# Optimization experiments

Measured on AMD Instinct MI355X. Metric: run time of the kernel, lower is better.

## Reference

```python
import jax, jax.numpy as jnp
import numpy as np

NUM_HEADS = 8  # matches init_kwargs num_heads
LN_EPS = 1e-5  # torch.nn.LayerNorm default


def setup_inputs() -> dict:
    key = jax.random.key(0)
    ks = jax.random.split(key, 12)
    E, B, H, S = 16384, 16, 256, 32
    edge_features = jax.random.normal(ks[0], (E, H), jnp.float32)
    edge_coords = jax.random.normal(ks[1], (E, 3), jnp.float32)
    # sorted, equal-size segments (all graphs non-empty)
    batch = jnp.repeat(jnp.arange(B, dtype=jnp.int32), E // B)
    s_h = 1.0 / np.sqrt(H)
    s_sh = 1.0 / np.sqrt(S * H)
    seed_vectors = jax.random.normal(ks[2], (S, H), jnp.float32)
    # weights stored [in, out] (transposed vs torch nn.Linear)
    Wq = jax.random.normal(ks[3], (H, H), jnp.float32) * s_h
    Wk = jax.random.normal(ks[4], (H, H), jnp.float32) * s_h
    Wv = jax.random.normal(ks[5], (H, H), jnp.float32) * s_h
    Wo = jax.random.normal(ks[6], (H, H), jnp.float32) * s_h
    bo = jnp.zeros((H,), jnp.float32)
    ln_g = jnp.ones((H,), jnp.float32)
    ln_b = jnp.zeros((H,), jnp.float32)
    W1 = jax.random.normal(ks[7], (S * H, H), jnp.float32) * s_sh
    b1 = jnp.zeros((H,), jnp.float32)
    W2 = jax.random.normal(ks[8], (H, H), jnp.float32) * s_h
    b2 = jnp.zeros((H,), jnp.float32)
    return dict(edge_features=edge_features, edge_coords=edge_coords, batch=batch,
                seed_vectors=seed_vectors, Wq=Wq, Wk=Wk, Wv=Wv, Wo=Wo, bo=bo,
                ln_g=ln_g, ln_b=ln_b, W1=W1, b1=b1, W2=W2, b2=b2, num_graphs=B)


def reference(edge_features, edge_coords, batch, seed_vectors, Wq, Wk, Wv, Wo, bo,
              ln_g, ln_b, W1, b1, W2, b2, num_graphs):
    S, H = seed_vectors.shape
    nh = NUM_HEADS
    hd = H // nh
    q = (seed_vectors @ Wq).reshape(S, nh, hd)          # shared across graphs
    k = (edge_features @ Wk).reshape(-1, nh, hd)        # [E, nh, hd]
    v = (edge_features @ Wv).reshape(-1, nh, hd)
    scores = jnp.einsum('shd,ehd->esh', q, k) / np.sqrt(hd).astype(np.float32)
    # segment softmax over edges within each graph
    m = jax.lax.stop_gradient(jax.ops.segment_max(scores, batch, num_segments=num_graphs))
    num = jnp.exp(scores - m[batch])
    den = jax.ops.segment_sum(num, batch, num_segments=num_graphs)
    w = num / den[batch]                                # [E, S, nh]
    att = jax.ops.segment_sum(jnp.einsum('esh,ehd->eshd', w, v), batch,
                              num_segments=num_graphs)  # [B, S, nh, hd]
    att = att.reshape(num_graphs, S, H)                 # concat heads (head-major)
    y = seed_vectors[None, :, :] + att @ Wo + bo        # residual + out_proj
    mu = jnp.mean(y, axis=-1, keepdims=True)
    var = jnp.mean((y - mu) ** 2, axis=-1, keepdims=True)
    y = (y - mu) / jnp.sqrt(var + LN_EPS) * ln_g + ln_b
    flat = y.reshape(num_graphs, S * H)
    h1 = jax.nn.silu(flat @ W1 + b1)
    return h1 @ W2 + b2                                 # [B, H]
```

## Files before the change

### kernel.cpp

```cpp
#include <hip/hip_runtime.h>
#include <math.h>
#include <stdint.h>

#define E_EDGES 16384
#define H_DIM   256
#define S_SEEDS 32
#define NHEADS  8
#define HDIM    32
#define BGRAPHS 16
#define EPG     1024
#define NCHUNK  256
#define CPG     16
#define RSQRT_HD 0.17677669529663687f

typedef __attribute__((ext_vector_type(8))) short bf16x8;
typedef __attribute__((ext_vector_type(4))) float f32x4;

__device__ inline unsigned short f2bf(float x) {
    unsigned u = __float_as_uint(x);
    u += 0x7fff + ((u >> 16) & 1);
    return (unsigned short)(u >> 16);
}
__device__ inline float bf2f(unsigned int h) {
    return __uint_as_float((h & 0xffffu) << 16);
}
__device__ inline unsigned pack2(float a, float b) {
    return (unsigned)f2bf(a) | ((unsigned)f2bf(b) << 16);
}

__global__ __launch_bounds__(256) void k_wc(const float* __restrict__ Wv,
                                            const float* __restrict__ Wk,
                                            const float* __restrict__ Wq,
                                            const float* __restrict__ seed,
                                            unsigned short* __restrict__ WcT) {
    int j = blockIdx.x;
    int i = threadIdx.x;
    float val;
    if (j < H_DIM) {
        val = Wv[i * H_DIM + j];
    } else {
        int c = j - H_DIM;
        int h = c >> 5, s = c & 31;
        __shared__ float qp[8][33];
        __shared__ float qrow[HDIM];
        int d = i & 31, g = i >> 5;
        const float* wq = &Wq[(g * 32) * H_DIM + h * HDIM + d];
        const float* sd = &seed[s * H_DIM + g * 32];
        float p = 0.f;
        #pragma unroll
        for (int ii = 0; ii < 32; ++ii)
            p = fmaf(sd[ii], wq[(size_t)ii * H_DIM], p);
        qp[g][d] = p;
        __syncthreads();
        if (i < HDIM) {
            float qv = 0.f;
            #pragma unroll
            for (int g2 = 0; g2 < 8; ++g2) qv += qp[g2][i];
            qrow[i] = qv;
        }
        __syncthreads();
        const float* wk = &Wk[i * H_DIM + h * HDIM];
        float acc = 0.f;
        #pragma unroll
        for (int dd = 0; dd < HDIM; dd += 4) {
            float4 w = *(const float4*)&wk[dd];
            float4 qq = *(const float4*)&qrow[dd];
            acc = fmaf(w.x, qq.x, acc); acc = fmaf(w.y, qq.y, acc);
            acc = fmaf(w.z, qq.z, acc); acc = fmaf(w.w, qq.w, acc);
        }
        val = acc * RSQRT_HD;
    }
    WcT[j * H_DIM + i] = f2bf(val);
}

struct HalfBuf {
    union {
        unsigned short Bs[2][128][40];
        unsigned short Pt[128][72];
    };
};
struct SMattn {
    unsigned short As[64][264];
    HalfBuf hb[2];
    unsigned short Vt[2][128][72];
    float smx[2][2][128];
    float ssm[2][2][128];
};

__global__ __launch_bounds__(512) void k_attn(const float* __restrict__ A,
                                              const unsigned short* __restrict__ WcT,
                                              float* __restrict__ outc,
                                              float* __restrict__ mg,
                                              float* __restrict__ sg) {
    __shared__ SMattn sm;
    int tid = threadIdx.x;
    int chunk = blockIdx.x;
    int e0 = chunk * 64;
    int half = tid >> 8;
    int tl = tid & 255;
    int w4 = tl >> 6, lane = tid & 63;
    int lr = lane & 15, kg = lane >> 4;
    int wm = (w4 & 1) * 32, wn = (w4 >> 1) * 64;

    {
        int r = tid >> 3, cg8 = tid & 7;
        const float* ap = &A[(size_t)(e0 + r) * H_DIM + cg8 * 32];
        #pragma unroll
        for (int i = 0; i < 4; ++i) {
            float4 x = *(const float4*)&ap[i * 8];
            float4 y = *(const float4*)&ap[i * 8 + 4];
            uint4 o;
            o.x = pack2(x.x, x.y); o.y = pack2(x.z, x.w);
            o.z = pack2(y.x, y.y); o.w = pack2(y.z, y.w);
            *(uint4*)&sm.As[r][cg8 * 32 + i * 8] = o;
        }
    }
    int brow = tl >> 1, bhalf16 = (tl & 1) * 16;
    f32x4 acc2[2][2] = {};
    uint4 pb0, pb1;
    {
        const unsigned short* bp = &WcT[(size_t)(half * 128 + brow) * H_DIM + bhalf16];
        pb0 = *(const uint4*)bp; pb1 = *(const uint4*)(bp + 8);
    }
    #pragma unroll
    for (int t2 = 0; t2 < 2; ++t2) {
        f32x4 acc[2][4] = {};
        #pragma unroll
        for (int k = 0; k < 8; ++k) {
            *(uint4*)&sm.hb[half].Bs[k & 1][brow][bhalf16]     = pb0;
            *(uint4*)&sm.hb[half].Bs[k & 1][brow][bhalf16 + 8] = pb1;
            __syncthreads();
            int nk = k + 1, nt2 = t2;
            if (nk == 8) { nk = 0; nt2 = t2 + 1; }
            if (nt2 < 2) {
                const unsigned short* bp =
                    &WcT[(size_t)(half * 128 + nt2 * 256 + brow) * H_DIM + nk * 32 + bhalf16];
                pb0 = *(const uint4*)bp; pb1 = *(const uint4*)(bp + 8);
            }
            bf16x8 af[2], bfv[4];
            #pragma unroll
            for (int mi = 0; mi < 2; ++mi)
                af[mi] = *(const bf16x8*)&sm.As[wm + mi * 16 + lr][k * 32 + kg * 8];
            #pragma unroll
            for (int ni = 0; ni < 4; ++ni)
                bfv[ni] = *(const bf16x8*)&sm.hb[half].Bs[k & 1][wn + ni * 16 + lr][kg * 8];
            #pragma unroll
            for (int mi = 0; mi < 2; ++mi)
                #pragma unroll
                for (int ni = 0; ni < 4; ++ni)
                    acc[mi][ni] = __builtin_amdgcn_mfma_f32_16x16x32_bf16(
                        af[mi], bfv[ni], acc[mi][ni], 0, 0, 0);
        }
        if (t2 == 0) {
            #pragma unroll
            for (int mi = 0; mi < 2; ++mi)
                #pragma unroll
                for (int ni = 0; ni < 4; ++ni)
                    #pragma unroll
                    for (int r = 0; r < 4; ++r)
                        sm.Vt[half][wn + ni * 16 + lr][wm + mi * 16 + kg * 4 + r] =
                            f2bf(acc[mi][ni][r]);
        } else {
            float tmax[4];
            #pragma unroll
            for (int ni = 0; ni < 4; ++ni) {
                float m = -1e30f;
                #pragma unroll
                for (int mi = 0; mi < 2; ++mi)
                    #pragma unroll
                    for (int r = 0; r < 4; ++r) m = fmaxf(m, acc[mi][ni][r]);
                m = fmaxf(m, __shfl_xor(m, 16, 64));
                m = fmaxf(m, __shfl_xor(m, 32, 64));
                tmax[ni] = m;
            }
            if (kg == 0) {
                #pragma unroll
                for (int ni = 0; ni < 4; ++ni)
                    sm.smx[half][w4 & 1][wn + ni * 16 + lr] = tmax[ni];
            }
            __syncthreads();
            float tsum[4];
            #pragma unroll
            for (int ni = 0; ni < 4; ++ni) {
                int col = wn + ni * 16 + lr;
                float m = fmaxf(sm.smx[half][0][col], sm.smx[half][1][col]);
                float sv = 0.f;
                #pragma unroll
                for (int mi = 0; mi < 2; ++mi)
                    #pragma unroll
                    for (int r = 0; r < 4; ++r) {
                        float e_ = __expf(acc[mi][ni][r] - m);
                        unsigned short eb = f2bf(e_);
                        sm.hb[half].Pt[col][wm + mi * 16 + kg * 4 + r] = eb;
                        sv += bf2f(eb);
                    }
                sv += __shfl_xor(sv, 16, 64);
                sv += __shfl_xor(sv, 32, 64);
                tsum[ni] = sv;
            }
            if (kg == 0) {
                #pragma unroll
                for (int ni = 0; ni < 4; ++ni)
                    sm.ssm[half][w4 & 1][wn + ni * 16 + lr] = tsum[ni];
            }
            __syncthreads();
            if (tl < 128) {
                float m = fmaxf(sm.smx[half][0][tl], sm.smx[half][1][tl]);
                float sv = sm.ssm[half][0][tl] + sm.ssm[half][1][tl];
                mg[(size_t)chunk * H_DIM + half * 128 + tl] = m;
                sg[(size_t)chunk * H_DIM + half * 128 + tl] = sv;
            }
            #pragma unroll
            for (int ms = 0; ms < 2; ++ms)
                #pragma unroll
                for (int nd = 0; nd < 2; ++nd)
                    #pragma unroll
                    for (int kk = 0; kk < 2; ++kk) {
                        bf16x8 pa = *(const bf16x8*)
                            &sm.hb[half].Pt[w4 * 32 + ms * 16 + lr][kk * 32 + kg * 8];
                        bf16x8 vb = *(const bf16x8*)
                            &sm.Vt[half][w4 * 32 + nd * 16 + lr][kk * 32 + kg * 8];
                        acc2[ms][nd] = __builtin_amdgcn_mfma_f32_16x16x32_bf16(
                            pa, vb, acc2[ms][nd], 0, 0, 0);
                    }
        }
    }
    #pragma unroll
    for (int ms = 0; ms < 2; ++ms)
        #pragma unroll
        for (int nd = 0; nd < 2; ++nd)
            #pragma unroll
            for (int r = 0; r < 4; ++r) {
                int s_ = ms * 16 + kg * 4 + r;
                int c_ = (half * 4 + w4) * 32 + nd * 16 + lr;
                outc[((size_t)chunk * 32 + s_) * H_DIM + c_] = acc2[ms][nd][r];
            }
}

__device__ inline float block_sum256(float v, float* red4) {
    for (int o = 32; o > 0; o >>= 1) v += __shfl_xor(v, o, 64);
    int wid = threadIdx.x >> 6;
    if ((threadIdx.x & 63) == 0) red4[wid] = v;
    __syncthreads();
    float r = red4[0] + red4[1] + red4[2] + red4[3];
    __syncthreads();
    return r;
}

__global__ __launch_bounds__(256) void k_proj_ln(const float* __restrict__ outc,
                                                 const float* __restrict__ mg,
                                                 const float* __restrict__ sg,
                                                 const float* __restrict__ seed,
                                                 const float* __restrict__ Wo,
                                                 const float* __restrict__ bo,
                                                 const float* __restrict__ ln_g,
                                                 const float* __restrict__ ln_b,
                                                 float* __restrict__ Y) {
    int bs0 = blockIdx.x * 4;
    int c = threadIdx.x;
    int b = bs0 >> 5;
    __shared__ float sscale[4][CPG][8];
    __shared__ float arow[4][H_DIM];
    __shared__ float red4[4];
    if (c < 32) {
        int r = c >> 3, hh = c & 7;
        int s_r = (bs0 + r) & 31;
        int sc = hh * 32 + s_r;
        float mj[CPG];
        float M = -1e30f;
        #pragma unroll
        for (int j = 0; j < CPG; ++j) {
            mj[j] = mg[(size_t)(b * CPG + j) * H_DIM + sc];
            M = fmaxf(M, mj[j]);
        }
        float Den = 0.f;
        #pragma unroll
        for (int j = 0; j < CPG; ++j)
            Den += sg[(size_t)(b * CPG + j) * H_DIM + sc] * __expf(mj[j] - M);
        float inv = 1.f / Den;
        #pragma unroll
        for (int j = 0; j < CPG; ++j)
            sscale[r][j][hh] = __expf(mj[j] - M) * inv;
    }
    __syncthreads();
    int h = c >> 5;
    #pragma unroll
    for (int r = 0; r < 4; ++r) {
        int s_r = (bs0 + r) & 31;
        float a = 0.f;
        #pragma unroll
        for (int j = 0; j < CPG; ++j)
            a = fmaf(outc[((size_t)(b * CPG + j) * 32 + s_r) * H_DIM + c],
                     sscale[r][j][h], a);
        arow[r][c] = a;
    }
    __syncthreads();
    float acc[4];
    float b0 = bo[c];
    #pragma unroll
    for (int r = 0; r < 4; ++r) acc[r] = b0;
    for (int i = 0; i < H_DIM; i += 4) {
        float4 a0 = *(const float4*)&arow[0][i];
        float4 a1 = *(const float4*)&arow[1][i];
        float4 a2 = *(const float4*)&arow[2][i];
        float4 a3 = *(const float4*)&arow[3][i];
        float w0 = Wo[(i + 0) * H_DIM + c], w1 = Wo[(i + 1) * H_DIM + c];
        float w2 = Wo[(i + 2) * H_DIM + c], w3 = Wo[(i + 3) * H_DIM + c];
        acc[0] = fmaf(a0.x, w0, acc[0]); acc[0] = fmaf(a0.y, w1, acc[0]);
        acc[0] = fmaf(a0.z, w2, acc[0]); acc[0] = fmaf(a0.w, w3, acc[0]);
        acc[1] = fmaf(a1.x, w0, acc[1]); acc[1] = fmaf(a1.y, w1, acc[1]);
        acc[1] = fmaf(a1.z, w2, acc[1]); acc[1] = fmaf(a1.w, w3, acc[1]);
        acc[2] = fmaf(a2.x, w0, acc[2]); acc[2] = fmaf(a2.y, w1, acc[2]);
        acc[2] = fmaf(a2.z, w2, acc[2]); acc[2] = fmaf(a2.w, w3, acc[2]);
        acc[3] = fmaf(a3.x, w0, acc[3]); acc[3] = fmaf(a3.y, w1, acc[3]);
        acc[3] = fmaf(a3.z, w2, acc[3]); acc[3] = fmaf(a3.w, w3, acc[3]);
    }
    float g = ln_g[c], be = ln_b[c];
    #pragma unroll
    for (int r = 0; r < 4; ++r) {
        int bs = bs0 + r;
        float y = seed[(bs & 31) * H_DIM + c] + acc[r];
        float mu = block_sum256(y, red4) * (1.f / 256.f);
        float d = y - mu;
        float var = block_sum256(d * d, red4) * (1.f / 256.f);
        Y[(size_t)bs * H_DIM + c] = d * rsqrtf(var + 1e-5f) * g + be;
    }
}

__global__ __launch_bounds__(256) void k_mlp1(const float* __restrict__ Y,
                                              const float* __restrict__ W1,
                                              float* __restrict__ part) {
    int ch = blockIdx.x;
    int c = threadIdx.x;
    int i0 = ch * 64;
    __shared__ float fbuf[16][64];
    #pragma unroll
    for (int it = 0; it < 4; ++it) {
        int li = it * 256 + c;
        fbuf[li >> 6][li & 63] = Y[(size_t)(li >> 6) * 8192 + i0 + (li & 63)];
    }
    __syncthreads();
    float acc[16];
    #pragma unroll
    for (int b = 0; b < 16; ++b) acc[b] = 0.f;
    for (int ii = 0; ii < 64; ++ii) {
        float w = W1[(size_t)(i0 + ii) * H_DIM + c];
        #pragma unroll
        for (int b = 0; b < 16; ++b) acc[b] = fmaf(fbuf[b][ii], w, acc[b]);
    }
    #pragma unroll
    for (int b = 0; b < 16; ++b)
        part[((size_t)b * 128 + ch) * H_DIM + c] = acc[b];
}

__global__ __launch_bounds__(256) void k_mlp2(const float* __restrict__ part,
                                              const float* __restrict__ b1,
                                              const float* __restrict__ W2,
                                              const float* __restrict__ b2,
                                              float* __restrict__ out) {
    int b = blockIdx.x;
    int c = threadIdx.x;
    float s = b1[c];
    const float* pb = &part[(size_t)b * 128 * H_DIM + c];
    #pragma unroll 4
    for (int ch = 0; ch < 128; ++ch) s += pb[(size_t)ch * H_DIM];
    float h1 = s / (1.f + __expf(-s));
    __shared__ float hrow[H_DIM];
    hrow[c] = h1;
    __syncthreads();
    float acc = b2[c];
    for (int j = 0; j < H_DIM; j += 4) {
        float4 hq = *(const float4*)&hrow[j];
        acc = fmaf(hq.x, W2[(j + 0) * H_DIM + c], acc);
        acc = fmaf(hq.y, W2[(j + 1) * H_DIM + c], acc);
        acc = fmaf(hq.z, W2[(j + 2) * H_DIM + c], acc);
        acc = fmaf(hq.w, W2[(j + 3) * H_DIM + c], acc);
    }
    out[(size_t)b * H_DIM + c] = acc;
}

extern "C" void kernel_launch(void* const* d_in, const int* in_sizes, int n_in,
                              void* d_out, int out_size, void* d_ws, size_t ws_size,
                              hipStream_t stream) {
    const float* edge_features = (const float*)d_in[0];
    const float* seed = (const float*)d_in[3];
    const float* Wq   = (const float*)d_in[4];
    const float* Wk   = (const float*)d_in[5];
    const float* Wv   = (const float*)d_in[6];
    const float* Wo   = (const float*)d_in[7];
    const float* bo   = (const float*)d_in[8];
    const float* ln_g = (const float*)d_in[9];
    const float* ln_b = (const float*)d_in[10];
    const float* W1   = (const float*)d_in[11];
    const float* b1   = (const float*)d_in[12];
    const float* W2   = (const float*)d_in[13];
    const float* b2   = (const float*)d_in[14];
    float* out = (float*)d_out;

    float* ws = (float*)d_ws;
    unsigned short* WcT = (unsigned short*)ws;
    float* outc = ws + 65536;
    float* mg   = outc + 2097152;
    float* sg   = mg + 65536;
    float* Y    = sg + 65536;
    float* part = Y + 131072;

    k_wc      <<<512, 256, 0, stream>>>(Wv, Wk, Wq, seed, WcT);
    k_attn    <<<NCHUNK, 512, 0, stream>>>(edge_features, WcT, outc, mg, sg);
    k_proj_ln <<<BGRAPHS * S_SEEDS / 4, 256, 0, stream>>>(outc, mg, sg, seed, Wo, bo, ln_g, ln_b, Y);
    k_mlp1    <<<128, 256, 0, stream>>>(Y, W1, part);
    k_mlp2    <<<BGRAPHS, 256, 0, stream>>>(part, b1, W2, b2, out);
}
```

Baseline: 152.9 us.

## Restructure attention GEMM so each wave owns 64 full columns with register-fed B

Reworks the k_attn tiling so each of 8 waves computes a 64x64 tile covering all 64 edges for its own 64 WcT columns, loading B fragments straight from global memory into a double-buffered register set instead of staging them through shared memory. Waves 0-3 produce V and waves 4-7 produce scores, so each score wave sees the full column and the softmax max/sum needs no cross-wave reduction. This removes the per-k-step barriers and the smx/ssm shared arrays. In exchange it uses more accumulator registers per wave, and WcT loads are strided per lane rather than cooperative.

```diff
diff --git a/kernel.cpp b/kernel.cpp
--- a/kernel.cpp
+++ b/kernel.cpp
@@ -73,18 +73,10 @@
     WcT[j * H_DIM + i] = f2bf(val);
 }
 
-struct HalfBuf {
-    union {
-        unsigned short Bs[2][128][40];
-        unsigned short Pt[128][72];
-    };
-};
 struct SMattn {
     unsigned short As[64][264];
-    HalfBuf hb[2];
-    unsigned short Vt[2][128][72];
-    float smx[2][2][128];
-    float ssm[2][2][128];
+    unsigned short Vt[256][72];
+    unsigned short Pt[256][72];
 };
 
 __global__ __launch_bounds__(512) void k_attn(const float* __restrict__ A,
@@ -96,11 +88,8 @@
     int tid = threadIdx.x;
     int chunk = blockIdx.x;
     int e0 = chunk * 64;
-    int half = tid >> 8;
-    int tl = tid & 255;
-    int w4 = tl >> 6, lane = tid & 63;
+    int w = tid >> 6, lane = tid & 63;
     int lr = lane & 15, kg = lane >> 4;
-    int wm = (w4 & 1) * 32, wn = (w4 >> 1) * 64;
 
     {
         int r = tid >> 3, cg8 = tid & 7;
@@ -115,116 +104,90 @@
             *(uint4*)&sm.As[r][cg8 * 32 + i * 8] = o;
         }
     }
-    int brow = tl >> 1, bhalf16 = (tl & 1) * 16;
+    __syncthreads();
+
+    const unsigned short* brow = &WcT[(size_t)(w * 64 + lr) * H_DIM + kg * 8];
+    uint4 bfr[2][4];
+    #pragma unroll
+    for (int ni = 0; ni < 4; ++ni) {
+        bfr[0][ni] = *(const uint4*)(brow + (size_t)ni * 16 * H_DIM);
+        bfr[1][ni] = *(const uint4*)(brow + (size_t)ni * 16 * H_DIM + 32);
+    }
+    f32x4 acc[4][4] = {};
+    #pragma unroll
+    for (int k = 0; k < 8; ++k) {
+        bf16x8 af[4], bv[4];
+        #pragma unroll
+        for (int mi = 0; mi < 4; ++mi)
+            af[mi] = *(const bf16x8*)&sm.As[mi * 16 + lr][k * 32 + kg * 8];
+        #pragma unroll
+        for (int ni = 0; ni < 4; ++ni)
+            bv[ni] = *(const bf16x8*)&bfr[k & 1][ni];
+        if (k < 6) {
+            #pragma unroll
+            for (int ni = 0; ni < 4; ++ni)
+                bfr[k & 1][ni] = *(const uint4*)(brow + (size_t)ni * 16 * H_DIM + (k + 2) * 32);
+        }
+        #pragma unroll
+        for (int mi = 0; mi < 4; ++mi)
+            #pragma unroll
+            for (int ni = 0; ni < 4; ++ni)
+                acc[mi][ni] = __builtin_amdgcn_mfma_f32_16x16x32_bf16(
+                    af[mi], bv[ni], acc[mi][ni], 0, 0, 0);
+    }
+
+    if (w < 4) {
+        #pragma unroll
+        for (int mi = 0; mi < 4; ++mi)
+            #pragma unroll
+            for (int ni = 0; ni < 4; ++ni)
+                #pragma unroll
+                for (int r = 0; r < 4; ++r)
+                    sm.Vt[w * 64 + ni * 16 + lr][mi * 16 + kg * 4 + r] =
+                        f2bf(acc[mi][ni][r]);
+    } else {
+        int wn = (w - 4) * 64;
+        #pragma unroll
+        for (int ni = 0; ni < 4; ++ni) {
+            float m = -1e30f;
+            #pragma unroll
+            for (int mi = 0; mi < 4; ++mi)
+                #pragma unroll
+                for (int r = 0; r < 4; ++r) m = fmaxf(m, acc[mi][ni][r]);
+            m = fmaxf(m, __shfl_xor(m, 16, 64));
+            m = fmaxf(m, __shfl_xor(m, 32, 64));
+            float sv = 0.f;
+            #pragma unroll
+            for (int mi = 0; mi < 4; ++mi)
+                #pragma unroll
+                for (int r = 0; r < 4; ++r) {
+                    float e_ = __expf(acc[mi][ni][r] - m);
+                    unsigned short eb = f2bf(e_);
+                    sm.Pt[wn + ni * 16 + lr][mi * 16 + kg * 4 + r] = eb;
+                    sv += bf2f(eb);
+                }
+            sv += __shfl_xor(sv, 16, 64);
+            sv += __shfl_xor(sv, 32, 64);
+            if (kg == 0) {
+                mg[(size_t)chunk * H_DIM + wn + ni * 16 + lr] = m;
+                sg[(size_t)chunk * H_DIM + wn + ni * 16 + lr] = sv;
+            }
+        }
+    }
+    __syncthreads();
+
     f32x4 acc2[2][2] = {};
-    uint4 pb0, pb1;
-    {
-        const unsigned short* bp = &WcT[(size_t)(half * 128 + brow) * H_DIM + bhalf16];
-        pb0 = *(const uint4*)bp; pb1 = *(const uint4*)(bp + 8);
-    }
-    #pragma unroll
-    for (int t2 = 0; t2 < 2; ++t2) {
-        f32x4 acc[2][4] = {};
-        #pragma unroll
-        for (int k = 0; k < 8; ++k) {
-            *(uint4*)&sm.hb[half].Bs[k & 1][brow][bhalf16]     = pb0;
-            *(uint4*)&sm.hb[half].Bs[k & 1][brow][bhalf16 + 8] = pb1;
-            __syncthreads();
-            int nk = k + 1, nt2 = t2;
-            if (nk == 8) { nk = 0; nt2 = t2 + 1; }
-            if (nt2 < 2) {
-                const unsigned short* bp =
-                    &WcT[(size_t)(half * 128 + nt2 * 256 + brow) * H_DIM + nk * 32 + bhalf16];
-                pb0 = *(const uint4*)bp; pb1 = *(const uint4*)(bp + 8);
+    #pragma unroll
+    for (int ms = 0; ms < 2; ++ms)
+        #pragma unroll
+        for (int nd = 0; nd < 2; ++nd)
+            #pragma unroll
+            for (int kk = 0; kk < 2; ++kk) {
+                bf16x8 pa = *(const bf16x8*)&sm.Pt[w * 32 + ms * 16 + lr][kk * 32 + kg * 8];
+                bf16x8 vb = *(const bf16x8*)&sm.Vt[w * 32 + nd * 16 + lr][kk * 32 + kg * 8];
+                acc2[ms][nd] = __builtin_amdgcn_mfma_f32_16x16x32_bf16(
+                    pa, vb, acc2[ms][nd], 0, 0, 0);
             }
-            bf16x8 af[2], bfv[4];
-            #pragma unroll
-            for (int mi = 0; mi < 2; ++mi)
-                af[mi] = *(const bf16x8*)&sm.As[wm + mi * 16 + lr][k * 32 + kg * 8];
-            #pragma unroll
-            for (int ni = 0; ni < 4; ++ni)
-                bfv[ni] = *(const bf16x8*)&sm.hb[half].Bs[k & 1][wn + ni * 16 + lr][kg * 8];
-            #pragma unroll
-            for (int mi = 0; mi < 2; ++mi)
-                #pragma unroll
-                for (int ni = 0; ni < 4; ++ni)
-                    acc[mi][ni] = __builtin_amdgcn_mfma_f32_16x16x32_bf16(
-                        af[mi], bfv[ni], acc[mi][ni], 0, 0, 0);
-        }
-        if (t2 == 0) {
-            #pragma unroll
-            for (int mi = 0; mi < 2; ++mi)
-                #pragma unroll
-                for (int ni = 0; ni < 4; ++ni)
-                    #pragma unroll
-                    for (int r = 0; r < 4; ++r)
-                        sm.Vt[half][wn + ni * 16 + lr][wm + mi * 16 + kg * 4 + r] =
-                            f2bf(acc[mi][ni][r]);
-        } else {
-            float tmax[4];
-            #pragma unroll
-            for (int ni = 0; ni < 4; ++ni) {
-                float m = -1e30f;
-                #pragma unroll
-                for (int mi = 0; mi < 2; ++mi)
-                    #pragma unroll
-                    for (int r = 0; r < 4; ++r) m = fmaxf(m, acc[mi][ni][r]);
-                m = fmaxf(m, __shfl_xor(m, 16, 64));
-                m = fmaxf(m, __shfl_xor(m, 32, 64));
-                tmax[ni] = m;
-            }
-            if (kg == 0) {
-                #pragma unroll
-                for (int ni = 0; ni < 4; ++ni)
-                    sm.smx[half][w4 & 1][wn + ni * 16 + lr] = tmax[ni];
-            }
-            __syncthreads();
-            float tsum[4];
-            #pragma unroll
-            for (int ni = 0; ni < 4; ++ni) {
-                int col = wn + ni * 16 + lr;
-                float m = fmaxf(sm.smx[half][0][col], sm.smx[half][1][col]);
-                float sv = 0.f;
-                #pragma unroll
-                for (int mi = 0; mi < 2; ++mi)
-                    #pragma unroll
-                    for (int r = 0; r < 4; ++r) {
-                        float e_ = __expf(acc[mi][ni][r] - m);
-                        unsigned short eb = f2bf(e_);
-                        sm.hb[half].Pt[col][wm + mi * 16 + kg * 4 + r] = eb;
-                        sv += bf2f(eb);
-                    }
-                sv += __shfl_xor(sv, 16, 64);
-                sv += __shfl_xor(sv, 32, 64);
-                tsum[ni] = sv;
-            }
-            if (kg == 0) {
-                #pragma unroll
-                for (int ni = 0; ni < 4; ++ni)
-                    sm.ssm[half][w4 & 1][wn + ni * 16 + lr] = tsum[ni];
-            }
-            __syncthreads();
-            if (tl < 128) {
-                float m = fmaxf(sm.smx[half][0][tl], sm.smx[half][1][tl]);
-                float sv = sm.ssm[half][0][tl] + sm.ssm[half][1][tl];
-                mg[(size_t)chunk * H_DIM + half * 128 + tl] = m;
-                sg[(size_t)chunk * H_DIM + half * 128 + tl] = sv;
-            }
-            #pragma unroll
-            for (int ms = 0; ms < 2; ++ms)
-                #pragma unroll
-                for (int nd = 0; nd < 2; ++nd)
-                    #pragma unroll
-                    for (int kk = 0; kk < 2; ++kk) {
-                        bf16x8 pa = *(const bf16x8*)
-                            &sm.hb[half].Pt[w4 * 32 + ms * 16 + lr][kk * 32 + kg * 8];
-                        bf16x8 vb = *(const bf16x8*)
-                            &sm.Vt[half][w4 * 32 + nd * 16 + lr][kk * 32 + kg * 8];
-                        acc2[ms][nd] = __builtin_amdgcn_mfma_f32_16x16x32_bf16(
-                            pa, vb, acc2[ms][nd], 0, 0, 0);
-                    }
-        }
-    }
     #pragma unroll
     for (int ms = 0; ms < 2; ++ms)
         #pragma unroll
@@ -232,7 +195,7 @@
             #pragma unroll
             for (int r = 0; r < 4; ++r) {
                 int s_ = ms * 16 + kg * 4 + r;
-                int c_ = (half * 4 + w4) * 32 + nd * 16 + lr;
+                int c_ = w * 32 + nd * 16 + lr;
                 outc[((size_t)chunk * 32 + s_) * H_DIM + c_] = acc2[ms][nd][r];
             }
 }
```

New measurement: 149.8 us. -2.0%, faster.
